# Kernel tuning notes

Hardware: AMD Instinct MI355X
Metric: run time of the kernel (lower is better)

Reference implementation:

```python
import jax, jax.numpy as jnp
import numpy as np

N, IN_DIM, HID, H1, NCLS, H2, E = 50000, 256, 32, 8, 16, 8, 800000


def gat_conv(x, edge_index, W, a_src, a_dst, b, H, C):
    """PyG-style GATConv, eval mode (attention dropout off), concat=True,
    negative_slope=0.2, add_self_loops=True."""
    n = x.shape[0]
    loop = jnp.arange(n)
    src = jnp.concatenate([edge_index[0], loop])  # [E+N]
    dst = jnp.concatenate([edge_index[1], loop])
    h = (x @ W).reshape(n, H, C)                  # [N,H,C]
    alpha_s = jnp.sum(h * a_src, axis=-1)         # [N,H]
    alpha_d = jnp.sum(h * a_dst, axis=-1)         # [N,H]
    e = jax.nn.leaky_relu(alpha_s[src] + alpha_d[dst], 0.2)  # [E+N,H]
    # segment softmax over incoming edges of each target node
    e_max = jax.ops.segment_max(e, dst, num_segments=n)      # [N,H] (self-loop guarantees nonempty)
    p = jnp.exp(e - e_max[dst])
    denom = jax.ops.segment_sum(p, dst, num_segments=n)
    alpha = p / (denom[dst] + 1e-16)              # [E+N,H]
    msg = h[src] * alpha[:, :, None]              # [E+N,H,C]
    out = jax.ops.segment_sum(msg, dst, num_segments=n)      # [N,H,C]
    return out.reshape(n, H * C) + b


def setup_inputs() -> dict:
    key = jax.random.key(0)
    ks = jax.random.split(key, 12)
    x = jax.random.normal(ks[0], (N, IN_DIM), dtype=jnp.float32)
    edge_index = jax.random.randint(ks[1], (2, E), 0, N, dtype=jnp.int64)
    s1 = 1.0 / np.sqrt(IN_DIM)
    s2 = 1.0 / np.sqrt(HID * H1)
    W1 = jax.random.normal(ks[2], (IN_DIM, H1 * HID), dtype=jnp.float32) * s1
    a_src1 = jax.random.normal(ks[3], (H1, HID), dtype=jnp.float32) * s1
    a_dst1 = jax.random.normal(ks[4], (H1, HID), dtype=jnp.float32) * s1
    b1 = jnp.zeros((H1 * HID,), dtype=jnp.float32)
    W2 = jax.random.normal(ks[5], (H1 * HID, H2 * NCLS), dtype=jnp.float32) * s2
    a_src2 = jax.random.normal(ks[6], (H2, NCLS), dtype=jnp.float32) * s2
    a_dst2 = jax.random.normal(ks[7], (H2, NCLS), dtype=jnp.float32) * s2
    b2 = jnp.zeros((H2 * NCLS,), dtype=jnp.float32)
    return {"x": x, "edge_index": edge_index, "W1": W1, "a_src1": a_src1,
            "a_dst1": a_dst1, "b1": b1, "W2": W2, "a_src2": a_src2,
            "a_dst2": a_dst2, "b2": b2}


def reference(x, edge_index, W1, a_src1, a_dst1, b1, W2, a_src2, a_dst2, b2):
    # eval mode: F.dropout is identity
    h = gat_conv(x, edge_index, W1, a_src1, a_dst1, b1, H1, HID)   # [N, H1*HID]
    h = jax.nn.elu(h)
    h = gat_conv(h, edge_index, W2, a_src2, a_dst2, b2, H2, NCLS)  # [N, H2*NCLS]
    return jax.nn.log_softmax(h, axis=1)
```

## Files before the change

### kernel.cpp

```cpp
#include <hip/hip_runtime.h>
#include <hip/hip_fp16.h>

#define NN 50000
#define NE 800000
#define NGRID1 782

typedef _Float16 half4v __attribute__((ext_vector_type(4)));
typedef _Float16 half8v __attribute__((ext_vector_type(8)));
typedef float f32x4 __attribute__((ext_vector_type(4)));

#define Q_SCALE 0.04724409448f
#define Q_INV   21.16666667f

#define CVTB0(f, w) asm("v_cvt_f32_ubyte0 %0, %1" : "=v"(f) : "v"(w))
#define CVTB1(f, w) asm("v_cvt_f32_ubyte1 %0, %1" : "=v"(f) : "v"(w))
#define CVTB2(f, w) asm("v_cvt_f32_ubyte2 %0, %1" : "=v"(f) : "v"(w))
#define CVTB3(f, w) asm("v_cvt_f32_ubyte3 %0, %1" : "=v"(f) : "v"(w))

static __device__ __forceinline__ float lrelu(float x) { return x > 0.f ? x : 0.2f * x; }

static __device__ __forceinline__ int detect64(const void* ei) {
  const unsigned* w = (const unsigned*)ei;
  return (w[1] | w[3] | w[5] | w[7]) == 0u;
}

static __device__ __forceinline__ int edge_at(const void* ei, int is64, long long idx) {
  if (is64) return (int)((const long long*)ei)[idx];
  return ((const int*)ei)[idx];
}

__global__ void count_prep_kernel(const void* __restrict__ ei, int* __restrict__ counts,
                                  const float* __restrict__ W1, const float* __restrict__ W2,
                                  const float* __restrict__ aS1, const float* __restrict__ aD1,
                                  const float* __restrict__ aS2, const float* __restrict__ aD2,
                                  _Float16* __restrict__ W1p, _Float16* __restrict__ W2p,
                                  _Float16* __restrict__ Wa1p, _Float16* __restrict__ Wa2p) {
  long long gid = (long long)blockIdx.x * blockDim.x + threadIdx.x;
  if (gid < NE) {
    int is64 = detect64(ei);
    int d = edge_at(ei, is64, (long long)NE + gid);
    atomicAdd(&counts[d], 1);
    return;
  }
  int i = (int)(gid - NE);
  if (i < 65536) {
    int j = i & 7, l = (i >> 3) & 63, kst = (i >> 9) & 7, ct = i >> 12;
    int col = ct * 16 + (l & 15);
    int k = kst * 32 + ((l >> 4) << 3) + j;
    W1p[i] = (_Float16)W1[(size_t)k * 256 + col];
  } else if (i < 98304) {
    int n = i - 65536;
    int j = n & 7, l = (n >> 3) & 63, kst = (n >> 9) & 7, ct = n >> 12;
    int col = ct * 16 + (l & 15);
    int k = kst * 32 + ((l >> 4) << 3) + j;
    W2p[n] = (_Float16)W2[(size_t)k * 128 + col];
  } else if (i < 102400) {
    int n = i - 98304;
    int j = n & 7, l = (n >> 3) & 63, kst = n >> 9;
    int row = l & 15;
    int head = row & 7;
    const float* a = (row < 8) ? aS1 : aD1;
    int k = kst * 32 + ((l >> 4) << 3) + j;
    float s = 0.f;
    #pragma unroll 8
    for (int c = 0; c < 32; ++c)
      s += W1[(size_t)k * 256 + head * 32 + c] * a[head * 32 + c];
    Wa1p[n] = (_Float16)s;
  } else if (i < 106496) {
    int n = i - 102400;
    int j = n & 7, l = (n >> 3) & 63, kst = n >> 9;
    int row = l & 15;
    int head = row & 7;
    const float* a = (row < 8) ? aS2 : aD2;
    int k = kst * 32 + ((l >> 4) << 3) + j;
    float s = 0.f;
    #pragma unroll 8
    for (int c = 0; c < 16; ++c)
      s += W2[(size_t)k * 128 + head * 16 + c] * a[head * 16 + c];
    Wa2p[n] = (_Float16)s;
  }
}

static __device__ __forceinline__ int block_scan_inc(int v, int tid) {
  __shared__ int ws[4];
  const int lane = tid & 63, wv = tid >> 6;
  #pragma unroll
  for (int off = 1; off < 64; off <<= 1) {
    int t = __shfl_up(v, off);
    if (lane >= off) v += t;
  }
  if (lane == 63) ws[wv] = v;
  __syncthreads();
  int add = 0;
  #pragma unroll
  for (int j = 0; j < 4; ++j) if (j < wv) add += ws[j];
  return v + add;
}

__global__ void scan1_kernel(const int* __restrict__ counts, int* __restrict__ bsums) {
  __shared__ int ws[4];
  const int tid = threadIdx.x;
  const int lane = tid & 63, wv = tid >> 6;
  int i = blockIdx.x * 256 + tid;
  int v = (i < NN) ? counts[i] : 0;
  #pragma unroll
  for (int off = 1; off < 64; off <<= 1) v += __shfl_xor(v, off);
  if (lane == 0) ws[wv] = v;
  __syncthreads();
  if (tid == 0) bsums[blockIdx.x] = ws[0] + ws[1] + ws[2] + ws[3];
}

__global__ void scan2_kernel(int* __restrict__ bsums, int nb) {
  const int tid = threadIdx.x;
  int v = (tid < nb) ? bsums[tid] : 0;
  int inc = block_scan_inc(v, tid);
  if (tid < nb) bsums[tid] = inc - v;
}

__global__ void scan3_kernel(const int* __restrict__ counts, const int* __restrict__ bsums,
                             int* __restrict__ rs) {
  const int tid = threadIdx.x;
  int i = blockIdx.x * 256 + tid;
  int v = (i < NN) ? counts[i] : 0;
  int inc = block_scan_inc(v, tid);
  if (i < NN) rs[i + 1] = bsums[blockIdx.x] + inc;
  if (i == 0) rs[0] = 0;
}

template<int BN, int NCF, bool A_Q8, bool Q8OUT>
static __device__ __forceinline__ void gemm_body(int bid, const void* __restrict__ Araw,
                                                 const _Float16* __restrict__ Bp,
                                                 const _Float16* __restrict__ Wap,
                                                 void* __restrict__ Cout,
                                                 float* __restrict__ alS,
                                                 float* __restrict__ alD, int M) {
  __shared__ __align__(16) _Float16 As[64][256 + 8];
  const int tid = threadIdx.x;
  const int bm0 = bid * 64;
  if (A_Q8) {
    const unsigned char* A8 = (const unsigned char*)Araw;
    #pragma unroll
    for (int t = 0; t < 2; ++t) {
      int idx = tid + t * 512;
      int r = idx >> 4, c16 = (idx & 15) << 4;
      int gr = bm0 + r;
      uint4 v = make_uint4(0x80808080u, 0x80808080u, 0x80808080u, 0x80808080u);
      if (gr < M) v = *(const uint4*)&A8[(size_t)gr * 256 + c16];
      unsigned dw[4] = { v.x, v.y, v.z, v.w };
      _Float16 hb[16];
      #pragma unroll
      for (int d = 0; d < 4; ++d) {
        float f0, f1, f2, f3;
        CVTB0(f0, dw[d]); CVTB1(f1, dw[d]); CVTB2(f2, dw[d]); CVTB3(f3, dw[d]);
        hb[4 * d + 0] = (_Float16)((f0 - 128.f) * Q_SCALE);
        hb[4 * d + 1] = (_Float16)((f1 - 128.f) * Q_SCALE);
        hb[4 * d + 2] = (_Float16)((f2 - 128.f) * Q_SCALE);
        hb[4 * d + 3] = (_Float16)((f3 - 128.f) * Q_SCALE);
      }
      *(half8v*)&As[r][c16] = *(half8v*)&hb[0];
      *(half8v*)&As[r][c16 + 8] = *(half8v*)&hb[8];
    }
  } else {
    const float* A = (const float*)Araw;
    #pragma unroll
    for (int g = 0; g < 2; ++g) {
      float4 tmp[4]; int rr[4], cc[4];
      #pragma unroll
      for (int t = 0; t < 4; ++t) {
        int idx = tid + (g * 4 + t) * 512;
        int r = idx >> 6, c4 = (idx & 63) << 2;
        int gr = bm0 + r;
        tmp[t] = make_float4(0.f, 0.f, 0.f, 0.f);
        if (gr < M) tmp[t] = *(const float4*)&A[(size_t)gr * 256 + c4];
        rr[t] = r; cc[t] = c4;
      }
      #pragma unroll
      for (int t = 0; t < 4; ++t) {
        half4v h = { (_Float16)tmp[t].x, (_Float16)tmp[t].y,
                     (_Float16)tmp[t].z, (_Float16)tmp[t].w };
        *(half4v*)&As[rr[t]][cc[t]] = h;
      }
    }
  }
  __syncthreads();
  const int lane = tid & 63, wv = tid >> 6;
  const int ncol0 = wv * (16 * NCF);
  const int lrow = lane & 15, lk8 = (lane >> 4) << 3;
  f32x4 acc[4][NCF];
  f32x4 acca[4];
  #pragma unroll
  for (int rf = 0; rf < 4; ++rf) {
    acca[rf] = (f32x4){0.f, 0.f, 0.f, 0.f};
    #pragma unroll
    for (int cf = 0; cf < NCF; ++cf) acc[rf][cf] = (f32x4){0.f, 0.f, 0.f, 0.f};
  }
  #pragma unroll
  for (int kst = 0; kst < 8; ++kst) {
    const int ks = kst * 32 + lk8;
    half8v af[4];
    #pragma unroll
    for (int rf = 0; rf < 4; ++rf)
      af[rf] = *(const half8v*)&As[16 * rf + lrow][ks];
    #pragma unroll
    for (int cf = 0; cf < NCF; ++cf) {
      half8v bf = *(const half8v*)&Bp[((size_t)((wv * NCF + cf) * 8 + kst) * 64 + lane) * 8];
      #pragma unroll
      for (int rf = 0; rf < 4; ++rf)
        acc[rf][cf] = __builtin_amdgcn_mfma_f32_16x16x32_f16(af[rf], bf, acc[rf][cf], 0, 0, 0);
    }
    if (wv == 0) {
      half8v bfa = *(const half8v*)&Wap[((size_t)kst * 64 + lane) * 8];
      #pragma unroll
      for (int rf = 0; rf < 4; ++rf)
        acca[rf] = __builtin_amdgcn_mfma_f32_16x16x32_f16(af[rf], bfa, acca[rf], 0, 0, 0);
    }
  }
  if (Q8OUT) {
    __syncthreads();
    constexpr int ROWB = BN + 16;
    char* Cs = (char*)&As[0][0];
    #pragma unroll
    for (int rf = 0; rf < 4; ++rf) {
      #pragma unroll
      for (int j = 0; j < 4; ++j) {
        int r = 16 * rf + 4 * ((lane >> 4) & 3) + j;
        #pragma unroll
        for (int cf = 0; cf < NCF; ++cf) {
          int col = ncol0 + 16 * cf + lrow;
          float v = acc[rf][cf][j];
          int q = __float2int_rn(fminf(fmaxf(v * Q_INV, -127.f), 127.f)) + 128;
          Cs[r * ROWB + col] = (char)q;
        }
      }
    }
    __syncthreads();
    unsigned char* C8 = (unsigned char*)Cout;
    for (int idx = tid; idx < 4 * BN; idx += 512) {
      int r = idx / (BN / 16), c16 = idx % (BN / 16);
      int grow = bm0 + r;
      if (grow < M)
        *(int4*)&C8[(size_t)grow * BN + 16 * c16] = *(const int4*)&Cs[r * ROWB + 16 * c16];
    }
  }
  if (wv == 0) {
    #pragma unroll
    for (int rf = 0; rf < 4; ++rf) {
      #pragma unroll
      for (int j = 0; j < 4; ++j) {
        int row = bm0 + 16 * rf + 4 * ((lane >> 4) & 3) + j;
        if (row < M) {
          float v = acca[rf][j];
          if (lrow < 8) alS[row * 8 + lrow] = v;
          else          alD[row * 8 + (lrow - 8)] = v;
        }
      }
    }
  }
}

__global__ __launch_bounds__(512) void gemm1_scatter_kernel(
    const void* __restrict__ Araw, const _Float16* __restrict__ Bp,
    const _Float16* __restrict__ Wap, void* __restrict__ Cout,
    float* __restrict__ alS, float* __restrict__ alD, int M,
    const void* __restrict__ ei, const int* __restrict__ rs,
    int* __restrict__ cursor, unsigned short* __restrict__ ssrc) {
  if (blockIdx.x < NGRID1) {
    gemm_body<256, 2, false, true>(blockIdx.x, Araw, Bp, Wap, Cout, alS, alD, M);
    return;
  }
  int e = (blockIdx.x - NGRID1) * 512 + threadIdx.x;
  if (e >= NE) return;
  int is64 = detect64(ei);
  int s = edge_at(ei, is64, e);
  int d = edge_at(ei, is64, (long long)NE + e);
  int p = atomicAdd(&cursor[d], 1);
  ssrc[rs[d] + p] = (unsigned short)s;
}

__global__ __launch_bounds__(512) void gemm2_kernel(
    const void* __restrict__ Araw, const _Float16* __restrict__ Bp,
    const _Float16* __restrict__ Wap, void* __restrict__ Cout,
    float* __restrict__ alS, float* __restrict__ alD, int M) {
  gemm_body<128, 1, true, true>(blockIdx.x, Araw, Bp, Wap, Cout, alS, alD, M);
}

#define ACCQ(w, p) do { \
    float f0_, f1_, f2_, f3_; \
    CVTB0(f0_, (w)); CVTB1(f1_, (w)); CVTB2(f2_, (w)); CVTB3(f3_, (w)); \
    ax0 += (p) * f0_; ax1 += (p) * f1_; ax2 += (p) * f2_; ax3 += (p) * f3_; \
  } while (0)

__global__ __launch_bounds__(256) void agg1_kernel(const unsigned char* __restrict__ h1q,
    const float* __restrict__ as, const float* __restrict__ ad,
    const int* __restrict__ rs, const unsigned short* __restrict__ ssrc,
    const float* __restrict__ bias, unsigned char* __restrict__ outq) {
  const int wid = (blockIdx.x * blockDim.x + threadIdx.x) >> 6;
  const int lane = threadIdx.x & 63;
  if (wid >= NN) return;
  const int node = wid;
  const int beg = rs[node], end = rs[node + 1];
  const int deg = end - beg;
  const int hd = lane >> 3;
  const float advh = ad[node * 8 + hd];
  const unsigned* hw = (const unsigned*)h1q;
  float denom = 0.f;
  float ax0 = 0.f, ax1 = 0.f, ax2 = 0.f, ax3 = 0.f;
  {
    float p = __expf(lrelu(as[node * 8 + hd] + advh));
    unsigned w = hw[(size_t)node * 64 + lane];
    ACCQ(w, p);
    denom = p;
  }
  const int gb = lane & 56;
  for (int base = 0; base < deg; base += 64) {
    const int cnt = min(deg - base, 64);
    int sv = (lane < cnt) ? (int)ssrc[beg + base + lane] : 0;
    int j = 0;
    for (; j + 8 <= cnt; j += 8) {
      int s0 = __builtin_amdgcn_readlane(sv, j + 0);
      int s1 = __builtin_amdgcn_readlane(sv, j + 1);
      int s2 = __builtin_amdgcn_readlane(sv, j + 2);
      int s3 = __builtin_amdgcn_readlane(sv, j + 3);
      int s4 = __builtin_amdgcn_readlane(sv, j + 4);
      int s5 = __builtin_amdgcn_readlane(sv, j + 5);
      int s6 = __builtin_amdgcn_readlane(sv, j + 6);
      int s7 = __builtin_amdgcn_readlane(sv, j + 7);
      unsigned w0 = hw[(size_t)s0 * 64 + lane];
      unsigned w1 = hw[(size_t)s1 * 64 + lane];
      unsigned w2 = hw[(size_t)s2 * 64 + lane];
      unsigned w3 = hw[(size_t)s3 * 64 + lane];
      unsigned w4 = hw[(size_t)s4 * 64 + lane];
      unsigned w5 = hw[(size_t)s5 * 64 + lane];
      unsigned w6 = hw[(size_t)s6 * 64 + lane];
      unsigned w7 = hw[(size_t)s7 * 64 + lane];
      int sl = __shfl(sv, j + (lane & 7));
      float pl = __expf(lrelu(as[(size_t)sl * 8 + hd] + advh));
      float p0 = __shfl(pl, gb + 0);
      float p1 = __shfl(pl, gb + 1);
      float p2 = __shfl(pl, gb + 2);
      float p3 = __shfl(pl, gb + 3);
      float p4 = __shfl(pl, gb + 4);
      float p5 = __shfl(pl, gb + 5);
      float p6 = __shfl(pl, gb + 6);
      float p7 = __shfl(pl, gb + 7);
      denom += (p0 + p1) + (p2 + p3) + ((p4 + p5) + (p6 + p7));
      ACCQ(w0, p0); ACCQ(w1, p1); ACCQ(w2, p2); ACCQ(w3, p3);
      ACCQ(w4, p4); ACCQ(w5, p5); ACCQ(w6, p6); ACCQ(w7, p7);
    }
    for (; j < cnt; ++j) {
      int s = __builtin_amdgcn_readlane(sv, j);
      float p = __expf(lrelu(as[s * 8 + hd] + advh));
      unsigned w = hw[(size_t)s * 64 + lane];
      ACCQ(w, p);
      denom += p;
    }
  }
  const float inv = 1.f / (denom + 1e-16f);
  const float4 bv = *(const float4*)&bias[lane * 4];
  float4 o;
  o.x = Q_SCALE * (ax0 * inv - 128.f) + bv.x;
  o.y = Q_SCALE * (ax1 * inv - 128.f) + bv.y;
  o.z = Q_SCALE * (ax2 * inv - 128.f) + bv.z;
  o.w = Q_SCALE * (ax3 * inv - 128.f) + bv.w;
  o.x = o.x > 0.f ? o.x : __expf(o.x) - 1.f;
  o.y = o.y > 0.f ? o.y : __expf(o.y) - 1.f;
  o.z = o.z > 0.f ? o.z : __expf(o.z) - 1.f;
  o.w = o.w > 0.f ? o.w : __expf(o.w) - 1.f;
  int q0 = __float2int_rn(fminf(fmaxf(o.x * Q_INV, -127.f), 127.f)) + 128;
  int q1 = __float2int_rn(fminf(fmaxf(o.y * Q_INV, -127.f), 127.f)) + 128;
  int q2 = __float2int_rn(fminf(fmaxf(o.z * Q_INV, -127.f), 127.f)) + 128;
  int q3 = __float2int_rn(fminf(fmaxf(o.w * Q_INV, -127.f), 127.f)) + 128;
  unsigned pk = (unsigned)q0 | ((unsigned)q1 << 8) | ((unsigned)q2 << 16) | ((unsigned)q3 << 24);
  ((unsigned*)outq)[(size_t)node * 64 + lane] = pk;
}

#define ACC2Q(w, p) do { \
    float f0_, f1_; \
    CVTB0(f0_, (w)); CVTB1(f1_, (w)); \
    ax0 += (p) * f0_; ax1 += (p) * f1_; \
  } while (0)

__global__ __launch_bounds__(256) void agg2_kernel(const unsigned char* __restrict__ h2q,
    const float* __restrict__ as, const float* __restrict__ ad,
    const int* __restrict__ rs, const unsigned short* __restrict__ ssrc,
    const float* __restrict__ bias, float* __restrict__ out) {
  const int wid = (blockIdx.x * blockDim.x + threadIdx.x) >> 6;
  const int lane = threadIdx.x & 63;
  if (wid >= NN) return;
  const int node = wid;
  const int beg = rs[node], end = rs[node + 1];
  const int deg = end - beg;
  const int hd = lane >> 3;
  const float advh = ad[node * 8 + hd];
  const unsigned short* hw = (const unsigned short*)h2q;
  float denom = 0.f;
  float ax0 = 0.f, ax1 = 0.f;
  {
    float p = __expf(lrelu(as[node * 8 + hd] + advh));
    unsigned w = hw[(size_t)node * 64 + lane];
    ACC2Q(w, p);
    denom = p;
  }
  const int gb = lane & 56;
  for (int base = 0; base < deg; base += 64) {
    const int cnt = min(deg - base, 64);
    int sv = (lane < cnt) ? (int)ssrc[beg + base + lane] : 0;
    int j = 0;
    for (; j + 8 <= cnt; j += 8) {
      int s0 = __builtin_amdgcn_readlane(sv, j + 0);
      int s1 = __builtin_amdgcn_readlane(sv, j + 1);
      int s2 = __builtin_amdgcn_readlane(sv, j + 2);
      int s3 = __builtin_amdgcn_readlane(sv, j + 3);
      int s4 = __builtin_amdgcn_readlane(sv, j + 4);
      int s5 = __builtin_amdgcn_readlane(sv, j + 5);
      int s6 = __builtin_amdgcn_readlane(sv, j + 6);
      int s7 = __builtin_amdgcn_readlane(sv, j + 7);
      unsigned w0 = hw[(size_t)s0 * 64 + lane];
      unsigned w1 = hw[(size_t)s1 * 64 + lane];
      unsigned w2 = hw[(size_t)s2 * 64 + lane];
      unsigned w3 = hw[(size_t)s3 * 64 + lane];
      unsigned w4 = hw[(size_t)s4 * 64 + lane];
      unsigned w5 = hw[(size_t)s5 * 64 + lane];
      unsigned w6 = hw[(size_t)s6 * 64 + lane];
      unsigned w7 = hw[(size_t)s7 * 64 + lane];
      int sl = __shfl(sv, j + (lane & 7));
      float pl = __expf(lrelu(as[(size_t)sl * 8 + hd] + advh));
      float p0 = __shfl(pl, gb + 0);
      float p1 = __shfl(pl, gb + 1);
      float p2 = __shfl(pl, gb + 2);
      float p3 = __shfl(pl, gb + 3);
      float p4 = __shfl(pl, gb + 4);
      float p5 = __shfl(pl, gb + 5);
      float p6 = __shfl(pl, gb + 6);
      float p7 = __shfl(pl, gb + 7);
      denom += (p0 + p1) + (p2 + p3) + ((p4 + p5) + (p6 + p7));
      ACC2Q(w0, p0); ACC2Q(w1, p1); ACC2Q(w2, p2); ACC2Q(w3, p3);
      ACC2Q(w4, p4); ACC2Q(w5, p5); ACC2Q(w6, p6); ACC2Q(w7, p7);
    }
    for (; j < cnt; ++j) {
      int s = __builtin_amdgcn_readlane(sv, j);
      float p = __expf(lrelu(as[s * 8 + hd] + advh));
      unsigned w = hw[(size_t)s * 64 + lane];
      ACC2Q(w, p);
      denom += p;
    }
  }
  const float inv = 1.f / (denom + 1e-16f);
  float v0 = Q_SCALE * (ax0 * inv - 128.f) + bias[lane * 2 + 0];
  float v1 = Q_SCALE * (ax1 * inv - 128.f) + bias[lane * 2 + 1];
  float mx = fmaxf(v0, v1);
  #pragma unroll
  for (int off = 1; off < 64; off <<= 1) mx = fmaxf(mx, __shfl_xor(mx, off));
  float sum = __expf(v0 - mx) + __expf(v1 - mx);
  #pragma unroll
  for (int off = 1; off < 64; off <<= 1) sum += __shfl_xor(sum, off);
  float lse = mx + __logf(sum);
  float2 o = make_float2(v0 - lse, v1 - lse);
  __builtin_nontemporal_store(o.x, &out[(size_t)node * 128 + lane * 2]);
  __builtin_nontemporal_store(o.y, &out[(size_t)node * 128 + lane * 2 + 1]);
}

extern "C" void kernel_launch(void* const* d_in, const int* in_sizes, int n_in,
                              void* d_out, int out_size, void* d_ws, size_t ws_size,
                              hipStream_t stream) {
  const float* x    = (const float*)d_in[0];
  const void*  ei   = d_in[1];
  const float* W1   = (const float*)d_in[2];
  const float* aS1  = (const float*)d_in[3];
  const float* aD1  = (const float*)d_in[4];
  const float* b1   = (const float*)d_in[5];
  const float* W2   = (const float*)d_in[6];
  const float* aS2  = (const float*)d_in[7];
  const float* aD2  = (const float*)d_in[8];
  const float* b2   = (const float*)d_in[9];
  float* out = (float*)d_out;

  char* ws = (char*)d_ws;
  unsigned char* h1q = (unsigned char*)ws; ws += (size_t)NN * 256;
  unsigned char* hmq = (unsigned char*)ws; ws += (size_t)NN * 256;
  unsigned char* h2q = (unsigned char*)ws; ws += (size_t)NN * 128;
  _Float16* W1p = (_Float16*)ws;       ws += (size_t)65536 * 2;
  _Float16* W2p = (_Float16*)ws;       ws += (size_t)32768 * 2;
  _Float16* Wa1p = (_Float16*)ws;      ws += (size_t)4096 * 2;
  _Float16* Wa2p = (_Float16*)ws;      ws += (size_t)4096 * 2;
  float* alS  = (float*)ws;            ws += (size_t)NN * 8 * 4;
  float* alD  = (float*)ws;            ws += (size_t)NN * 8 * 4;
  int* counts = (int*)ws;              ws += (size_t)NN * 4;
  int* cursor = (int*)ws;              ws += (size_t)NN * 4;
  int* rs     = (int*)ws;              ws += (size_t)(NN + 1) * 4;
  int* bsums  = (int*)ws;              ws += (size_t)256 * 4;
  unsigned short* ssrc = (unsigned short*)ws; ws += (size_t)NE * 2;

  const int NB = (NN + 255) / 256;

  hipMemsetAsync(counts, 0, (size_t)2 * NN * 4, stream);

  const long long total_cp = (long long)NE + 106496;
  count_prep_kernel<<<(int)((total_cp + 255) / 256), 256, 0, stream>>>(
      ei, counts, W1, W2, aS1, aD1, aS2, aD2, W1p, W2p, Wa1p, Wa2p);

  scan1_kernel<<<NB, 256, 0, stream>>>(counts, bsums);
  scan2_kernel<<<1, 256, 0, stream>>>(bsums, NB);
  scan3_kernel<<<NB, 256, 0, stream>>>(counts, bsums, rs);

  const int sgrid = (NE + 511) / 512;
  gemm1_scatter_kernel<<<NGRID1 + sgrid, 512, 0, stream>>>(
      x, W1p, Wa1p, h1q, alS, alD, NN, ei, rs, cursor, ssrc);

  agg1_kernel<<<(NN + 3) / 4, 256, 0, stream>>>(h1q, alS, alD, rs, ssrc, b1, hmq);

  gemm2_kernel<<<NGRID1, 512, 0, stream>>>(hmq, W2p, Wa2p, h2q, alS, alD, NN);
  agg2_kernel<<<(NN + 3) / 4, 256, 0, stream>>>(h2q, alS, alD, rs, ssrc, b2, out);
}
```

Baseline: 197.2 us.

## Replace per-node CSR scatter atomics with two-level bucketed scatter

The edge scatter no longer does one global atomic per destination node. Edges are first binned into 64-node buckets using a small global cursor array, and each record packs the source id with the destination's low 6 bits. A new kernel then places each bucket's records into final CSR order using shared-memory atomics. The goal is fewer scattered global atomics and cursor cache lines, at the cost of an extra kernel launch and an extra 3.2MB record buffer that must be written and read back.

Measured after the change: 352.7 us. +78.8%, slower.

```diff
diff --git a/kernel.cpp b/kernel.cpp
--- a/kernel.cpp
+++ b/kernel.cpp
@@ -4,6 +4,7 @@
 #define NN 50000
 #define NE 800000
 #define NGRID1 782
+#define NBKT 782
 
 typedef _Float16 half4v __attribute__((ext_vector_type(4)));
 typedef _Float16 half8v __attribute__((ext_vector_type(8)));
@@ -263,7 +264,7 @@
     const _Float16* __restrict__ Wap, void* __restrict__ Cout,
     float* __restrict__ alS, float* __restrict__ alD, int M,
     const void* __restrict__ ei, const int* __restrict__ rs,
-    int* __restrict__ cursor, unsigned short* __restrict__ ssrc) {
+    int* __restrict__ bcursor, unsigned* __restrict__ rec) {
   if (blockIdx.x < NGRID1) {
     gemm_body<256, 2, false, true>(blockIdx.x, Araw, Bp, Wap, Cout, alS, alD, M);
     return;
@@ -273,8 +274,28 @@
   int is64 = detect64(ei);
   int s = edge_at(ei, is64, e);
   int d = edge_at(ei, is64, (long long)NE + e);
-  int p = atomicAdd(&cursor[d], 1);
-  ssrc[rs[d] + p] = (unsigned short)s;
+  int b = d >> 6;
+  int pos = rs[b << 6] + atomicAdd(&bcursor[b], 1);
+  rec[pos] = (unsigned)s | ((unsigned)(d & 63) << 16);
+}
+
+__global__ __launch_bounds__(256) void binfix_kernel(const unsigned* __restrict__ rec,
+                                                     const int* __restrict__ rs,
+                                                     unsigned short* __restrict__ ssrc) {
+  __shared__ int cur[64];
+  const int b = blockIdx.x;
+  const int d0 = b << 6;
+  if (threadIdx.x < 64) cur[threadIdx.x] = 0;
+  __syncthreads();
+  const int beg = rs[d0];
+  const int endn = min(d0 + 64, NN);
+  const int end = rs[endn];
+  for (int i = beg + threadIdx.x; i < end; i += 256) {
+    unsigned r = rec[i];
+    int dlo = (r >> 16) & 63;
+    int p = atomicAdd(&cur[dlo], 1);
+    ssrc[rs[d0 + dlo] + p] = (unsigned short)(r & 0xffffu);
+  }
 }
 
 __global__ __launch_bounds__(512) void gemm2_kernel(
@@ -486,14 +507,15 @@
   float* alS  = (float*)ws;            ws += (size_t)NN * 8 * 4;
   float* alD  = (float*)ws;            ws += (size_t)NN * 8 * 4;
   int* counts = (int*)ws;              ws += (size_t)NN * 4;
-  int* cursor = (int*)ws;              ws += (size_t)NN * 4;
+  int* bcursor = (int*)ws;             ws += (size_t)1024 * 4;
   int* rs     = (int*)ws;              ws += (size_t)(NN + 1) * 4;
   int* bsums  = (int*)ws;              ws += (size_t)256 * 4;
+  unsigned* rec = (unsigned*)ws;       ws += (size_t)NE * 4;
   unsigned short* ssrc = (unsigned short*)ws; ws += (size_t)NE * 2;
 
   const int NB = (NN + 255) / 256;
 
-  hipMemsetAsync(counts, 0, (size_t)2 * NN * 4, stream);
+  hipMemsetAsync(counts, 0, (size_t)(NN + 1024) * 4, stream);
 
   const long long total_cp = (long long)NE + 106496;
   count_prep_kernel<<<(int)((total_cp + 255) / 256), 256, 0, stream>>>(
@@ -505,7 +527,9 @@
 
   const int sgrid = (NE + 511) / 512;
   gemm1_scatter_kernel<<<NGRID1 + sgrid, 512, 0, stream>>>(
-      x, W1p, Wa1p, h1q, alS, alD, NN, ei, rs, cursor, ssrc);
+      x, W1p, Wa1p, h1q, alS, alD, NN, ei, rs, bcursor, rec);
+
+  binfix_kernel<<<NBKT, 256, 0, stream>>>(rec, rs, ssrc);
 
   agg1_kernel<<<(NN + 3) / 4, 256, 0, stream>>>(h1q, alS, alD, rs, ssrc, b1, hmq);
 
```
